# Optimization experiments

Hardware: AMD Instinct MI355X
Metric: run time of the kernel (lower is better)

The kernel has to match this reference:

```python
import jax, jax.numpy as jnp
import numpy as np

B, C, H, W = 64, 64, 56, 56
MID = 2 * C  # two output nodes concatenated
EPS = 1e-5


def _conv1x1(x, w):
    # x: [B,C,H,W], w: [O,C] (1x1 conv kernel squeezed)
    return jnp.einsum('bchw,oc->bohw', x, w)


def _bn(x, g, b, m, v):
    # eval-mode BatchNorm2d with running stats
    sc = g * jax.lax.rsqrt(v + EPS)
    return x * sc[None, :, None, None] + (b - m * sc)[None, :, None, None]


def _maxpool3(x):
    # MaxPool2d(kernel=3, stride=1, padding=1)
    return jax.lax.reduce_window(x, -jnp.inf, jax.lax.max,
                                 (1, 1, 3, 3), (1, 1, 1, 1),
                                 [(0, 0), (0, 0), (1, 1), (1, 1)])


def _avgpool3(x):
    # AvgPool2d(kernel=3, stride=1, padding=1), count_include_pad=True -> /9
    s = jax.lax.reduce_window(x, 0.0, jax.lax.add,
                              (1, 1, 3, 3), (1, 1, 1, 1),
                              [(0, 0), (0, 0), (1, 1), (1, 1)])
    return s * (1.0 / 9.0)


def setup_inputs() -> dict:
    key = jax.random.key(0)
    ks = jax.random.split(key, 11)
    x = jax.random.normal(ks[0], (B, C, H, W), dtype=jnp.float32)
    w1 = jax.random.normal(ks[1], (C, C), dtype=jnp.float32) * 0.1
    w2 = jax.random.normal(ks[2], (C, MID), dtype=jnp.float32) * 0.1
    bn1_g = 1.0 + 0.1 * jax.random.normal(ks[3], (C,), dtype=jnp.float32)
    bn1_b = 0.1 * jax.random.normal(ks[4], (C,), dtype=jnp.float32)
    bn1_m = 0.1 * jax.random.normal(ks[5], (C,), dtype=jnp.float32)
    bn1_v = jax.random.uniform(ks[6], (C,), minval=0.5, maxval=1.5, dtype=jnp.float32)
    bn2_g = 1.0 + 0.1 * jax.random.normal(ks[7], (C,), dtype=jnp.float32)
    bn2_b = 0.1 * jax.random.normal(ks[8], (C,), dtype=jnp.float32)
    bn2_m = 0.1 * jax.random.normal(ks[9], (C,), dtype=jnp.float32)
    bn2_v = jax.random.uniform(ks[10], (C,), minval=0.5, maxval=1.5, dtype=jnp.float32)
    return dict(x=x, w1=w1, w2=w2,
                bn1_g=bn1_g, bn1_b=bn1_b, bn1_m=bn1_m, bn1_v=bn1_v,
                bn2_g=bn2_g, bn2_b=bn2_b, bn2_m=bn2_m, bn2_v=bn2_v)


def reference(x, w1, w2, bn1_g, bn1_b, bn1_m, bn1_v, bn2_g, bn2_b, bn2_m, bn2_v):
    # DAG g = [[[0,1],[1,2]], [[4,3],[3]], [[5,3],[3,100]], [[4,3],[100]]]
    # topoSort order: [0, 2, 1, 3]; output nodes (ordered): [2, 3]
    node0 = jax.nn.relu(_bn(_conv1x1(x, w1), bn1_g, bn1_b, bn1_m, bn1_v))
    node1 = _maxpool3(node0)            # op type 4, pred {0}
    node2 = _avgpool3(node0)            # op type 5, pred {0}
    node3 = _maxpool3(node1) + _maxpool3(node2)  # op type 4, preds {1,2}, summed
    cat = jnp.concatenate([node2, node3], axis=1)  # [B, 2C, H, W]
    out = jax.nn.relu(_bn(_conv1x1(cat, w2), bn2_g, bn2_b, bn2_m, bn2_v))
    return out
```

## Files before the change

### kernel.cpp

```cpp
#include <hip/hip_runtime.h>
#include <cstddef>

#define EPS 1e-5f
static constexpr int Bn = 64, Cn = 64, Hn = 56, Wn = 56, HWn = Hn * Wn;

typedef __attribute__((ext_vector_type(8))) short short8;
typedef __attribute__((ext_vector_type(8))) unsigned short ushort8;
typedef __attribute__((ext_vector_type(4))) float floatx4;
typedef __attribute__((ext_vector_type(16))) float floatx16;
typedef __attribute__((ext_vector_type(4))) unsigned int uintx4;
typedef __attribute__((ext_vector_type(2))) unsigned int uintx2;

__device__ __forceinline__ unsigned pack_rne(float a, float b) {
    unsigned ua = __float_as_uint(a), ub = __float_as_uint(b);
    ua = ua + 0x7fffu + ((ua >> 16) & 1u);
    ub = ub + 0x7fffu + ((ub >> 16) & 1u);
    return __builtin_amdgcn_perm(ub, ua, 0x07060302);
}
__device__ __forceinline__ unsigned pack_trunc(float a, float b) {
    return __builtin_amdgcn_perm(__float_as_uint(b), __float_as_uint(a), 0x07060302);
}
__device__ __forceinline__ ushort8 pmax(ushort8 a, ushort8 b) {
    return __builtin_elementwise_max(a, b);
}
__device__ __forceinline__ float bf_lo(unsigned u) { return __uint_as_float(u << 16); }
__device__ __forceinline__ float bf_hi(unsigned u) { return __uint_as_float(u & 0xffff0000u); }


__global__ __launch_bounds__(256) void k1_conv1(
    const float* __restrict__ x, const float* __restrict__ w1,
    const float* __restrict__ bg, const float* __restrict__ bb,
    const float* __restrict__ bm, const float* __restrict__ bv,
    unsigned short* __restrict__ node0)
{
    __shared__ float scs[64], shs[64];
    const int tid = threadIdx.x;
    if (tid < 64) {
        float sc = bg[tid] * rsqrtf(bv[tid] + EPS);
        scs[tid] = sc;
        shs[tid] = bb[tid] - bm[tid] * sc;
    }
    __syncthreads();
    const int lane = tid & 63;
    const int wv   = tid >> 6;
    const int m    = lane & 15;
    const int quad = lane >> 4;

    short8 afr[4][2];
    float shv[16];
    #pragma unroll
    for (int t = 0; t < 4; ++t) {
        const float sc = scs[t * 16 + m];
        #pragma unroll
        for (int kk = 0; kk < 2; ++kk) {
            const float* wp = w1 + (t * 16 + m) * 64 + kk * 32 + quad * 8;
            floatx4 f0 = *(const floatx4*)wp;
            floatx4 f1 = *(const floatx4*)(wp + 4);
            uintx4 u;
            u.x = pack_rne(f0[0] * sc, f0[1] * sc);
            u.y = pack_rne(f0[2] * sc, f0[3] * sc);
            u.z = pack_rne(f1[0] * sc, f1[1] * sc);
            u.w = pack_rne(f1[2] * sc, f1[3] * sc);
            afr[t][kk] = *(short8*)&u;
        }
        #pragma unroll
        for (int i = 0; i < 4; ++i) shv[t * 4 + i] = shs[t * 16 + quad * 4 + i];
    }

    #pragma unroll 1
    for (int tt = 0; tt < 4; ++tt) {
        const long P0 = (long)blockIdx.x * 256 + tt * 64;
        const int b = (int)(P0 / HWn);
        const int p0 = (int)(P0 - (long)b * HWn);
        const int p = p0 + wv * 16 + m;

        floatx4 acc[4];
        #pragma unroll
        for (int t = 0; t < 4; ++t) acc[t] = (floatx4){0.f, 0.f, 0.f, 0.f};

        #pragma unroll
        for (int kk = 0; kk < 2; ++kk) {
            float xv[8];
            #pragma unroll
            for (int j = 0; j < 8; ++j)
                xv[j] = x[(size_t)(b * 64 + kk * 32 + quad * 8 + j) * HWn + p];
            uintx4 u;
            u.x = pack_trunc(xv[0], xv[1]);
            u.y = pack_trunc(xv[2], xv[3]);
            u.z = pack_trunc(xv[4], xv[5]);
            u.w = pack_trunc(xv[6], xv[7]);
            short8 bfr = *(short8*)&u;
            #pragma unroll
            for (int t = 0; t < 4; ++t)
                acc[t] = __builtin_amdgcn_mfma_f32_16x16x32_bf16(afr[t][kk], bfr, acc[t], 0, 0, 0);
        }

        const int chunkbase = (quad >> 1);
        const int j0 = (quad & 1) * 4;
        #pragma unroll
        for (int t = 0; t < 4; ++t) {
            float v0 = acc[t][0] + shv[t * 4 + 0]; v0 = v0 > 0.f ? v0 : 0.f;
            float v1 = acc[t][1] + shv[t * 4 + 1]; v1 = v1 > 0.f ? v1 : 0.f;
            float v2 = acc[t][2] + shv[t * 4 + 2]; v2 = v2 > 0.f ? v2 : 0.f;
            float v3 = acc[t][3] + shv[t * 4 + 3]; v3 = v3 > 0.f ? v3 : 0.f;
            uintx2 st;
            st.x = pack_rne(v0, v1);
            st.y = pack_rne(v2, v3);
            int chunk = t * 2 + chunkbase;
            *(uintx2*)(node0 + ((size_t)(b * 8 + chunk) * HWn + p0 + wv * 16 + m) * 8 + j0) = st;
        }
    }
}

__global__ __launch_bounds__(256) void k2_pools(
    const unsigned short* __restrict__ node0, unsigned short* __restrict__ cat)
{
    const int tid = threadIdx.x;
    const int lane = tid & 63;
    const int wv = tid >> 6;
    const int bid = blockIdx.x;
    const int half = bid & 1;
    const int band = (bid >> 1) % 7;
    const int b = bid / 14;
    const int chunk = half * 4 + wv;
    const int lo = band * 8;
    const int col = lane;
    const bool act = col < Wn;
    const unsigned short* base = node0 + ((size_t)(b * 8 + chunk) * HWn) * 8;
    unsigned short* cavg = cat + ((size_t)(b * 16 + chunk) * HWn) * 8;
    unsigned short* cmax = cat + ((size_t)(b * 16 + 8 + chunk) * HWn) * 8;

    const ushort8 zz = (ushort8)0;
    float hs1[8], hs2[8];
    ushort8 h5a = zz, h5b = zz, h5c = zz, h5d = zz, nh1 = zz, nh2 = zz;
    #pragma unroll
    for (int j = 0; j < 8; ++j) hs1[j] = hs2[j] = 0.f;

    #pragma unroll
    for (int r = lo - 2; r <= lo + 9; ++r) {
        ushort8 d[5];
        #pragma unroll
        for (int dd = 0; dd < 5; ++dd) {
            int cc = col + dd - 2;
            bool ok = act && ((unsigned)cc < (unsigned)Wn) && ((unsigned)r < (unsigned)Hn);
            d[dd] = ok ? *(const ushort8*)(base + (size_t)(r * Wn + cc) * 8) : zz;
        }
        ushort8 hm5 = pmax(pmax(pmax(d[0], d[1]), pmax(d[2], d[3])), d[4]);
        ushort8 m5 = pmax(pmax(pmax(h5a, h5b), pmax(h5c, h5d)), hm5);
        h5a = h5b; h5b = h5c; h5c = h5d; h5d = hm5;

        const uintx4 ul = *(const uintx4*)&d[1];
        const uintx4 uv = *(const uintx4*)&d[2];
        const uintx4 ur = *(const uintx4*)&d[3];
        float a2[8];
        const int r2 = r - 1, r3 = r - 2;
        const bool v2 = (unsigned)r2 < (unsigned)Hn;
        #pragma unroll
        for (int w = 0; w < 4; ++w) {
            float l0 = bf_lo(ul[w]), l1 = bf_hi(ul[w]);
            float c0 = bf_lo(uv[w]), c1 = bf_hi(uv[w]);
            float r0 = bf_lo(ur[w]), r1 = bf_hi(ur[w]);
            float hsum0 = l0 + c0 + r0;
            float hsum1 = l1 + c1 + r1;
            a2[w * 2 + 0] = v2 ? (hs2[w * 2 + 0] + hs1[w * 2 + 0] + hsum0) * (1.f / 9.f) : 0.f;
            a2[w * 2 + 1] = v2 ? (hs2[w * 2 + 1] + hs1[w * 2 + 1] + hsum1) * (1.f / 9.f) : 0.f;
            hs2[w * 2 + 0] = hs1[w * 2 + 0]; hs1[w * 2 + 0] = hsum0;
            hs2[w * 2 + 1] = hs1[w * 2 + 1]; hs1[w * 2 + 1] = hsum1;
        }
        uintx4 ap;
        ap.x = pack_rne(a2[0], a2[1]);
        ap.y = pack_rne(a2[2], a2[3]);
        ap.z = pack_rne(a2[4], a2[5]);
        ap.w = pack_rne(a2[6], a2[7]);
        uintx4 al, ar;
        #pragma unroll
        for (int w = 0; w < 4; ++w) {
            unsigned u = ap[w];
            unsigned lu = __shfl_up(u, 1);
            unsigned ru = __shfl_down(u, 1);
            al[w] = (lane == 0) ? 0u : lu;
            ar[w] = (lane == 63) ? 0u : ru;
        }
        ushort8 nh = pmax(pmax(*(ushort8*)&al, *(ushort8*)&ap), *(ushort8*)&ar);
        ushort8 m3 = pmax(pmax(nh2, nh1), nh);
        nh2 = nh1; nh1 = nh;

        if (act && r2 >= lo && r2 < lo + 8)
            *(uintx4*)(cavg + (size_t)(r2 * Wn + col) * 8) = ap;
        if (act && r3 >= lo && r3 < lo + 8) {
            const uintx4 u5 = *(const uintx4*)&m5;
            const uintx4 u3 = *(const uintx4*)&m3;
            uintx4 st;
            #pragma unroll
            for (int w = 0; w < 4; ++w)
                st[w] = pack_rne(bf_lo(u5[w]) + bf_lo(u3[w]), bf_hi(u5[w]) + bf_hi(u3[w]));
            *(uintx4*)(cmax + (size_t)(r3 * Wn + col) * 8) = st;
        }
    }
}

__global__ __launch_bounds__(256) void k3_conv2(
    const unsigned short* __restrict__ cat, const float* __restrict__ w2,
    const float* __restrict__ bg, const float* __restrict__ bb,
    const float* __restrict__ bm, const float* __restrict__ bv,
    float* __restrict__ out)
{
    __shared__ unsigned short wl[1024 * 8];
    __shared__ float scs[64], shs[64];
    const int tid = threadIdx.x;
    if (tid < 64) {
        float sc = bg[tid] * rsqrtf(bv[tid] + EPS);
        scs[tid] = sc;
        shs[tid] = bb[tid] - bm[tid] * sc;
    }
    #pragma unroll
    for (int q = 0; q < 4; ++q) {
        int ci = tid * 4 + q;
        int lane_ = ci & 63, tk = ci >> 6;
        int t = tk >> 3, kt = tk & 7, n_ = lane_ & 31, h_ = lane_ >> 5;
        const float* wp = w2 + (t * 32 + n_) * 128 + kt * 16 + h_ * 8;
        floatx4 f0 = *(const floatx4*)wp;
        floatx4 f1 = *(const floatx4*)(wp + 4);
        uintx4 u;
        u.x = pack_rne(f0[0], f0[1]);
        u.y = pack_rne(f0[2], f0[3]);
        u.z = pack_rne(f1[0], f1[1]);
        u.w = pack_rne(f1[2], f1[3]);
        *(uintx4*)(wl + (size_t)ci * 8) = u;
    }
    __syncthreads();

    const int lane = tid & 63;
    const int wv = tid >> 6;
    const int n = lane & 31;
    const int h = lane >> 5;

    short8 afr[2][8];
    #pragma unroll
    for (int t = 0; t < 2; ++t)
        #pragma unroll
        for (int kt = 0; kt < 8; ++kt)
            afr[t][kt] = *(const short8*)(wl + ((size_t)((t * 8 + kt) * 64 + lane)) * 8);

    #pragma unroll 1
    for (int s = 0; s < 2; ++s) {
        const int tile = (blockIdx.x * 4 + wv) * 2 + s;
        const int b = tile / 98;
        const int p0 = (tile - b * 98) * 32;

        floatx16 acc0, acc1;
        #pragma unroll
        for (int i = 0; i < 16; ++i) { acc0[i] = 0.f; acc1[i] = 0.f; }

        #pragma unroll
        for (int kt = 0; kt < 8; ++kt) {
            short8 bfr = *(const short8*)(cat + ((size_t)(b * 16 + kt * 2 + h) * HWn + p0 + n) * 8);
            acc0 = __builtin_amdgcn_mfma_f32_32x32x16_bf16(afr[0][kt], bfr, acc0, 0, 0, 0);
            acc1 = __builtin_amdgcn_mfma_f32_32x32x16_bf16(afr[1][kt], bfr, acc1, 0, 0, 0);
        }

        float* ob = out + (size_t)b * 64 * HWn + p0 + n;
        #pragma unroll
        for (int r = 0; r < 16; ++r) {
            int o = (r & 3) + 8 * (r >> 2) + 4 * h;
            float v0 = fmaf(acc0[r], scs[o], shs[o]);
            ob[(size_t)o * HWn] = v0 > 0.f ? v0 : 0.f;
            float v1 = fmaf(acc1[r], scs[o + 32], shs[o + 32]);
            ob[(size_t)(o + 32) * HWn] = v1 > 0.f ? v1 : 0.f;
        }
    }
}

extern "C" void kernel_launch(void* const* d_in, const int* in_sizes, int n_in,
                              void* d_out, int out_size, void* d_ws, size_t ws_size,
                              hipStream_t stream)
{
    const float* x   = (const float*)d_in[0];
    const float* w1  = (const float*)d_in[1];
    const float* w2  = (const float*)d_in[2];
    const float* b1g = (const float*)d_in[3];
    const float* b1b = (const float*)d_in[4];
    const float* b1m = (const float*)d_in[5];
    const float* b1v = (const float*)d_in[6];
    const float* b2g = (const float*)d_in[7];
    const float* b2b = (const float*)d_in[8];
    const float* b2m = (const float*)d_in[9];
    const float* b2v = (const float*)d_in[10];

    float* out = (float*)d_out;
    unsigned short* node0 = (unsigned short*)d_ws;
    unsigned short* cat   = node0 + (size_t)Bn * HWn * 64;

    k1_conv1<<<dim3(784), dim3(256), 0, stream>>>(x, w1, b1g, b1b, b1m, b1v, node0);
    k2_pools<<<dim3(Bn * 14), dim3(256), 0, stream>>>(node0, cat);
    k3_conv2<<<dim3(784), dim3(256), 0, stream>>>(cat, w2, b2g, b2b, b2m, b2v, out);
}
```

Before: 165.4 us.

## Fuse pooling stage into second 1x1 conv through shared-memory concat tile

Merges the pooling kernel and the second conv kernel into one kernel. Each 512-thread block computes the avg and max-sum pools for a 4-row band of one image across all 8 channel chunks, writing the concatenated activations into a padded LDS tile. Seven waves then run the MFMA conv directly from LDS. This drops the global round trip of the 128-channel cat tensor and one launch. In exchange, the halo rows are recomputed per smaller band (8 rows loaded for 4 output rows), the LDS footprint is large, and one wave idles during the conv phase.

```diff
diff --git a/kernel.cpp b/kernel.cpp
--- a/kernel.cpp
+++ b/kernel.cpp
@@ -3,6 +3,7 @@
 
 #define EPS 1e-5f
 static constexpr int Bn = 64, Cn = 64, Hn = 56, Wn = 56, HWn = Hn * Wn;
+static constexpr int CSTR = 136;
 
 typedef __attribute__((ext_vector_type(8))) short short8;
 typedef __attribute__((ext_vector_type(8))) unsigned short ushort8;
@@ -112,99 +113,13 @@
     }
 }
 
-__global__ __launch_bounds__(256) void k2_pools(
-    const unsigned short* __restrict__ node0, unsigned short* __restrict__ cat)
-{
-    const int tid = threadIdx.x;
-    const int lane = tid & 63;
-    const int wv = tid >> 6;
-    const int bid = blockIdx.x;
-    const int half = bid & 1;
-    const int band = (bid >> 1) % 7;
-    const int b = bid / 14;
-    const int chunk = half * 4 + wv;
-    const int lo = band * 8;
-    const int col = lane;
-    const bool act = col < Wn;
-    const unsigned short* base = node0 + ((size_t)(b * 8 + chunk) * HWn) * 8;
-    unsigned short* cavg = cat + ((size_t)(b * 16 + chunk) * HWn) * 8;
-    unsigned short* cmax = cat + ((size_t)(b * 16 + 8 + chunk) * HWn) * 8;
-
-    const ushort8 zz = (ushort8)0;
-    float hs1[8], hs2[8];
-    ushort8 h5a = zz, h5b = zz, h5c = zz, h5d = zz, nh1 = zz, nh2 = zz;
-    #pragma unroll
-    for (int j = 0; j < 8; ++j) hs1[j] = hs2[j] = 0.f;
-
-    #pragma unroll
-    for (int r = lo - 2; r <= lo + 9; ++r) {
-        ushort8 d[5];
-        #pragma unroll
-        for (int dd = 0; dd < 5; ++dd) {
-            int cc = col + dd - 2;
-            bool ok = act && ((unsigned)cc < (unsigned)Wn) && ((unsigned)r < (unsigned)Hn);
-            d[dd] = ok ? *(const ushort8*)(base + (size_t)(r * Wn + cc) * 8) : zz;
-        }
-        ushort8 hm5 = pmax(pmax(pmax(d[0], d[1]), pmax(d[2], d[3])), d[4]);
-        ushort8 m5 = pmax(pmax(pmax(h5a, h5b), pmax(h5c, h5d)), hm5);
-        h5a = h5b; h5b = h5c; h5c = h5d; h5d = hm5;
-
-        const uintx4 ul = *(const uintx4*)&d[1];
-        const uintx4 uv = *(const uintx4*)&d[2];
-        const uintx4 ur = *(const uintx4*)&d[3];
-        float a2[8];
-        const int r2 = r - 1, r3 = r - 2;
-        const bool v2 = (unsigned)r2 < (unsigned)Hn;
-        #pragma unroll
-        for (int w = 0; w < 4; ++w) {
-            float l0 = bf_lo(ul[w]), l1 = bf_hi(ul[w]);
-            float c0 = bf_lo(uv[w]), c1 = bf_hi(uv[w]);
-            float r0 = bf_lo(ur[w]), r1 = bf_hi(ur[w]);
-            float hsum0 = l0 + c0 + r0;
-            float hsum1 = l1 + c1 + r1;
-            a2[w * 2 + 0] = v2 ? (hs2[w * 2 + 0] + hs1[w * 2 + 0] + hsum0) * (1.f / 9.f) : 0.f;
-            a2[w * 2 + 1] = v2 ? (hs2[w * 2 + 1] + hs1[w * 2 + 1] + hsum1) * (1.f / 9.f) : 0.f;
-            hs2[w * 2 + 0] = hs1[w * 2 + 0]; hs1[w * 2 + 0] = hsum0;
-            hs2[w * 2 + 1] = hs1[w * 2 + 1]; hs1[w * 2 + 1] = hsum1;
-        }
-        uintx4 ap;
-        ap.x = pack_rne(a2[0], a2[1]);
-        ap.y = pack_rne(a2[2], a2[3]);
-        ap.z = pack_rne(a2[4], a2[5]);
-        ap.w = pack_rne(a2[6], a2[7]);
-        uintx4 al, ar;
-        #pragma unroll
-        for (int w = 0; w < 4; ++w) {
-            unsigned u = ap[w];
-            unsigned lu = __shfl_up(u, 1);
-            unsigned ru = __shfl_down(u, 1);
-            al[w] = (lane == 0) ? 0u : lu;
-            ar[w] = (lane == 63) ? 0u : ru;
-        }
-        ushort8 nh = pmax(pmax(*(ushort8*)&al, *(ushort8*)&ap), *(ushort8*)&ar);
-        ushort8 m3 = pmax(pmax(nh2, nh1), nh);
-        nh2 = nh1; nh1 = nh;
-
-        if (act && r2 >= lo && r2 < lo + 8)
-            *(uintx4*)(cavg + (size_t)(r2 * Wn + col) * 8) = ap;
-        if (act && r3 >= lo && r3 < lo + 8) {
-            const uintx4 u5 = *(const uintx4*)&m5;
-            const uintx4 u3 = *(const uintx4*)&m3;
-            uintx4 st;
-            #pragma unroll
-            for (int w = 0; w < 4; ++w)
-                st[w] = pack_rne(bf_lo(u5[w]) + bf_lo(u3[w]), bf_hi(u5[w]) + bf_hi(u3[w]));
-            *(uintx4*)(cmax + (size_t)(r3 * Wn + col) * 8) = st;
-        }
-    }
-}
-
-__global__ __launch_bounds__(256) void k3_conv2(
-    const unsigned short* __restrict__ cat, const float* __restrict__ w2,
+__global__ __launch_bounds__(512, 4) void k23_fused(
+    const unsigned short* __restrict__ node0, const float* __restrict__ w2,
     const float* __restrict__ bg, const float* __restrict__ bb,
     const float* __restrict__ bm, const float* __restrict__ bv,
     float* __restrict__ out)
 {
+    __shared__ unsigned short ct[224 * CSTR];
     __shared__ unsigned short wl[1024 * 8];
     __shared__ float scs[64], shs[64];
     const int tid = threadIdx.x;
@@ -214,8 +129,8 @@
         shs[tid] = bb[tid] - bm[tid] * sc;
     }
     #pragma unroll
-    for (int q = 0; q < 4; ++q) {
-        int ci = tid * 4 + q;
+    for (int q = 0; q < 2; ++q) {
+        int ci = tid * 2 + q;
         int lane_ = ci & 63, tk = ci >> 6;
         int t = tk >> 3, kt = tk & 7, n_ = lane_ & 31, h_ = lane_ >> 5;
         const float* wp = w2 + (t * 32 + n_) * 128 + kt * 16 + h_ * 8;
@@ -228,10 +143,88 @@
         u.w = pack_rne(f1[2], f1[3]);
         *(uintx4*)(wl + (size_t)ci * 8) = u;
     }
-    __syncthreads();
 
     const int lane = tid & 63;
     const int wv = tid >> 6;
+    const int b = blockIdx.x / 14;
+    const int band = blockIdx.x % 14;
+    const int lo = band * 4;
+    const int col = lane;
+    const bool act = col < Wn;
+    const unsigned short* base = node0 + ((size_t)(b * 8 + wv) * HWn) * 8;
+
+    {
+        const ushort8 zz = (ushort8)0;
+        float hs1[8], hs2[8];
+        ushort8 h5a = zz, h5b = zz, h5c = zz, h5d = zz, nh1 = zz, nh2 = zz;
+        #pragma unroll
+        for (int j = 0; j < 8; ++j) hs1[j] = hs2[j] = 0.f;
+
+        #pragma unroll
+        for (int r = lo - 2; r <= lo + 5; ++r) {
+            ushort8 d[5];
+            #pragma unroll
+            for (int dd = 0; dd < 5; ++dd) {
+                int cc = col + dd - 2;
+                bool ok = act && ((unsigned)cc < (unsigned)Wn) && ((unsigned)r < (unsigned)Hn);
+                d[dd] = ok ? *(const ushort8*)(base + (size_t)(r * Wn + cc) * 8) : zz;
+            }
+            ushort8 hm5 = pmax(pmax(pmax(d[0], d[1]), pmax(d[2], d[3])), d[4]);
+            ushort8 m5 = pmax(pmax(pmax(h5a, h5b), pmax(h5c, h5d)), hm5);
+            h5a = h5b; h5b = h5c; h5c = h5d; h5d = hm5;
+
+            const uintx4 ul = *(const uintx4*)&d[1];
+            const uintx4 uv = *(const uintx4*)&d[2];
+            const uintx4 ur = *(const uintx4*)&d[3];
+            float a2[8];
+            const int r2 = r - 1, r3 = r - 2;
+            const bool v2 = (unsigned)r2 < (unsigned)Hn;
+            #pragma unroll
+            for (int w = 0; w < 4; ++w) {
+                float hsum0 = bf_lo(ul[w]) + bf_lo(uv[w]) + bf_lo(ur[w]);
+                float hsum1 = bf_hi(ul[w]) + bf_hi(uv[w]) + bf_hi(ur[w]);
+                a2[w * 2 + 0] = v2 ? (hs2[w * 2 + 0] + hs1[w * 2 + 0] + hsum0) * (1.f / 9.f) : 0.f;
+                a2[w * 2 + 1] = v2 ? (hs2[w * 2 + 1] + hs1[w * 2 + 1] + hsum1) * (1.f / 9.f) : 0.f;
+                hs2[w * 2 + 0] = hs1[w * 2 + 0]; hs1[w * 2 + 0] = hsum0;
+                hs2[w * 2 + 1] = hs1[w * 2 + 1]; hs1[w * 2 + 1] = hsum1;
+            }
+            uintx4 ap;
+            ap.x = pack_rne(a2[0], a2[1]);
+            ap.y = pack_rne(a2[2], a2[3]);
+            ap.z = pack_rne(a2[4], a2[5]);
+            ap.w = pack_rne(a2[6], a2[7]);
+            uintx4 al, ar;
+            #pragma unroll
+            for (int w = 0; w < 4; ++w) {
+                unsigned u = ap[w];
+                unsigned lu = __shfl_up(u, 1);
+                unsigned ru = __shfl_down(u, 1);
+                al[w] = (lane == 0) ? 0u : lu;
+                ar[w] = (lane == 63) ? 0u : ru;
+            }
+            ushort8 nh = pmax(pmax(*(ushort8*)&al, *(ushort8*)&ap), *(ushort8*)&ar);
+            ushort8 m3 = pmax(pmax(nh2, nh1), nh);
+            nh2 = nh1; nh1 = nh;
+
+            if (act && r2 >= lo && r2 < lo + 4) {
+                int px = (r2 - lo) * Wn + col;
+                *(uintx4*)(ct + (size_t)px * CSTR + wv * 8) = ap;
+            }
+            if (act && r3 >= lo && r3 < lo + 4) {
+                const uintx4 u5 = *(const uintx4*)&m5;
+                const uintx4 u3 = *(const uintx4*)&m3;
+                uintx4 st;
+                #pragma unroll
+                for (int w = 0; w < 4; ++w)
+                    st[w] = pack_rne(bf_lo(u5[w]) + bf_lo(u3[w]), bf_hi(u5[w]) + bf_hi(u3[w]));
+                int px = (r3 - lo) * Wn + col;
+                *(uintx4*)(ct + (size_t)px * CSTR + 64 + wv * 8) = st;
+            }
+        }
+    }
+    __syncthreads();
+
+    if (wv >= 7) return;
     const int n = lane & 31;
     const int h = lane >> 5;
 
@@ -242,32 +235,26 @@
         for (int kt = 0; kt < 8; ++kt)
             afr[t][kt] = *(const short8*)(wl + ((size_t)((t * 8 + kt) * 64 + lane)) * 8);
 
-    #pragma unroll 1
-    for (int s = 0; s < 2; ++s) {
-        const int tile = (blockIdx.x * 4 + wv) * 2 + s;
-        const int b = tile / 98;
-        const int p0 = (tile - b * 98) * 32;
-
-        floatx16 acc0, acc1;
-        #pragma unroll
-        for (int i = 0; i < 16; ++i) { acc0[i] = 0.f; acc1[i] = 0.f; }
-
-        #pragma unroll
-        for (int kt = 0; kt < 8; ++kt) {
-            short8 bfr = *(const short8*)(cat + ((size_t)(b * 16 + kt * 2 + h) * HWn + p0 + n) * 8);
-            acc0 = __builtin_amdgcn_mfma_f32_32x32x16_bf16(afr[0][kt], bfr, acc0, 0, 0, 0);
-            acc1 = __builtin_amdgcn_mfma_f32_32x32x16_bf16(afr[1][kt], bfr, acc1, 0, 0, 0);
-        }
-
-        float* ob = out + (size_t)b * 64 * HWn + p0 + n;
-        #pragma unroll
-        for (int r = 0; r < 16; ++r) {
-            int o = (r & 3) + 8 * (r >> 2) + 4 * h;
-            float v0 = fmaf(acc0[r], scs[o], shs[o]);
-            ob[(size_t)o * HWn] = v0 > 0.f ? v0 : 0.f;
-            float v1 = fmaf(acc1[r], scs[o + 32], shs[o + 32]);
-            ob[(size_t)(o + 32) * HWn] = v1 > 0.f ? v1 : 0.f;
-        }
+    const int px0 = wv * 32;
+    floatx16 acc0, acc1;
+    #pragma unroll
+    for (int i = 0; i < 16; ++i) { acc0[i] = 0.f; acc1[i] = 0.f; }
+
+    #pragma unroll
+    for (int kt = 0; kt < 8; ++kt) {
+        short8 bfr = *(const short8*)(ct + (size_t)(px0 + n) * CSTR + kt * 16 + h * 8);
+        acc0 = __builtin_amdgcn_mfma_f32_32x32x16_bf16(afr[0][kt], bfr, acc0, 0, 0, 0);
+        acc1 = __builtin_amdgcn_mfma_f32_32x32x16_bf16(afr[1][kt], bfr, acc1, 0, 0, 0);
+    }
+
+    float* ob = out + (size_t)b * 64 * HWn + lo * Wn + px0 + n;
+    #pragma unroll
+    for (int r = 0; r < 16; ++r) {
+        int o = (r & 3) + 8 * (r >> 2) + 4 * h;
+        float v0 = fmaf(acc0[r], scs[o], shs[o]);
+        ob[(size_t)o * HWn] = v0 > 0.f ? v0 : 0.f;
+        float v1 = fmaf(acc1[r], scs[o + 32], shs[o + 32]);
+        ob[(size_t)(o + 32) * HWn] = v1 > 0.f ? v1 : 0.f;
     }
 }
 
@@ -289,9 +276,7 @@
 
     float* out = (float*)d_out;
     unsigned short* node0 = (unsigned short*)d_ws;
-    unsigned short* cat   = node0 + (size_t)Bn * HWn * 64;
 
     k1_conv1<<<dim3(784), dim3(256), 0, stream>>>(x, w1, b1g, b1b, b1m, b1v, node0);
-    k2_pools<<<dim3(Bn * 14), dim3(256), 0, stream>>>(node0, cat);
-    k3_conv2<<<dim3(784), dim3(256), 0, stream>>>(cat, w2, b2g, b2b, b2m, b2v, out);
-}
+    k23_fused<<<dim3(Bn * 14), dim3(512), 0, stream>>>(node0, w2, b2g, b2b, b2m, b2v, out);
+}
```

Measured after the change: 170.6 us. 1.03x slower.

## Stage conv1 input through double-buffered LDS and prefetch rows in pooling kernel

Applied to the files above, without the earlier changes.

Conv1 now loads each 64-pixel x tile with coalesced float4 global loads into a register stage, transposes it into a padded LDS buffer, and double-buffers so the next tile's global load overlaps the current tile's MFMA work. This replaces the earlier strided scalar per-channel global loads. The pooling kernel software-prefetches the next row's five neighbour loads before processing the current row. The conv2 tile loop is also fully unrolled. The cost is extra LDS use, barriers, and register pressure.

```diff
diff --git a/kernel.cpp b/kernel.cpp
--- a/kernel.cpp
+++ b/kernel.cpp
@@ -3,6 +3,7 @@
 
 #define EPS 1e-5f
 static constexpr int Bn = 64, Cn = 64, Hn = 56, Wn = 56, HWn = Hn * Wn;
+static constexpr int XS = 65;
 
 typedef __attribute__((ext_vector_type(8))) short short8;
 typedef __attribute__((ext_vector_type(8))) unsigned short ushort8;
@@ -33,6 +34,7 @@
     const float* __restrict__ bm, const float* __restrict__ bv,
     unsigned short* __restrict__ node0)
 {
+    __shared__ float xs[2][64 * XS];
     __shared__ float scs[64], shs[64];
     const int tid = threadIdx.x;
     if (tid < 64) {
@@ -45,6 +47,7 @@
     const int wv   = tid >> 6;
     const int m    = lane & 15;
     const int quad = lane >> 4;
+    const int qoff = quad * 8;
 
     short8 afr[4][2];
     float shv[16];
@@ -53,7 +56,7 @@
         const float sc = scs[t * 16 + m];
         #pragma unroll
         for (int kk = 0; kk < 2; ++kk) {
-            const float* wp = w1 + (t * 16 + m) * 64 + kk * 32 + quad * 8;
+            const float* wp = w1 + (t * 16 + m) * 64 + kk * 32 + qoff;
             floatx4 f0 = *(const floatx4*)wp;
             floatx4 f1 = *(const floatx4*)(wp + 4);
             uintx4 u;
@@ -67,12 +70,39 @@
         for (int i = 0; i < 4; ++i) shv[t * 4 + i] = shs[t * 16 + quad * 4 + i];
     }
 
-    #pragma unroll 1
+    floatx4 stg[4];
+    auto ldtile = [&](int tt) {
+        const int P = blockIdx.x * 256 + tt * 64;
+        const int b = P / HWn, p0 = P - b * HWn;
+        #pragma unroll
+        for (int q = 0; q < 4; ++q) {
+            int idx = q * 256 + tid;
+            int c = idx >> 4, f = idx & 15;
+            stg[q] = *(const floatx4*)(x + (size_t)(b * 64 + c) * HWn + p0 + f * 4);
+        }
+    };
+    auto sttile = [&](int buf) {
+        #pragma unroll
+        for (int q = 0; q < 4; ++q) {
+            int idx = q * 256 + tid;
+            int c = idx >> 4, f = idx & 15;
+            #pragma unroll
+            for (int k = 0; k < 4; ++k)
+                xs[buf][(f * 4 + k) * XS + c] = stg[q][k];
+        }
+    };
+
+    ldtile(0);
+    sttile(0);
+
+    #pragma unroll
     for (int tt = 0; tt < 4; ++tt) {
-        const long P0 = (long)blockIdx.x * 256 + tt * 64;
-        const int b = (int)(P0 / HWn);
-        const int p0 = (int)(P0 - (long)b * HWn);
-        const int p = p0 + wv * 16 + m;
+        __syncthreads();
+        if (tt < 3) ldtile(tt + 1);
+
+        const int P = blockIdx.x * 256 + tt * 64;
+        const int b = P / HWn, p0 = P - b * HWn;
+        const float* xr = &xs[tt & 1][(wv * 16 + m) * XS];
 
         floatx4 acc[4];
         #pragma unroll
@@ -80,15 +110,14 @@
 
         #pragma unroll
         for (int kk = 0; kk < 2; ++kk) {
-            float xv[8];
+            float f[8];
             #pragma unroll
-            for (int j = 0; j < 8; ++j)
-                xv[j] = x[(size_t)(b * 64 + kk * 32 + quad * 8 + j) * HWn + p];
+            for (int j = 0; j < 8; ++j) f[j] = xr[kk * 32 + qoff + j];
             uintx4 u;
-            u.x = pack_trunc(xv[0], xv[1]);
-            u.y = pack_trunc(xv[2], xv[3]);
-            u.z = pack_trunc(xv[4], xv[5]);
-            u.w = pack_trunc(xv[6], xv[7]);
+            u.x = pack_trunc(f[0], f[1]);
+            u.y = pack_trunc(f[2], f[3]);
+            u.z = pack_trunc(f[4], f[5]);
+            u.w = pack_trunc(f[6], f[7]);
             short8 bfr = *(short8*)&u;
             #pragma unroll
             for (int t = 0; t < 4; ++t)
@@ -109,6 +138,8 @@
             int chunk = t * 2 + chunkbase;
             *(uintx2*)(node0 + ((size_t)(b * 8 + chunk) * HWn + p0 + wv * 16 + m) * 8 + j0) = st;
         }
+
+        if (tt < 3) sttile((tt + 1) & 1);
     }
 }
 
@@ -131,20 +162,29 @@
     unsigned short* cmax = cat + ((size_t)(b * 16 + 8 + chunk) * HWn) * 8;
 
     const ushort8 zz = (ushort8)0;
-    float hs1[8], hs2[8];
-    ushort8 h5a = zz, h5b = zz, h5c = zz, h5d = zz, nh1 = zz, nh2 = zz;
-    #pragma unroll
-    for (int j = 0; j < 8; ++j) hs1[j] = hs2[j] = 0.f;
-
-    #pragma unroll
-    for (int r = lo - 2; r <= lo + 9; ++r) {
-        ushort8 d[5];
+    auto load5 = [&](int r, ushort8* d) {
         #pragma unroll
         for (int dd = 0; dd < 5; ++dd) {
             int cc = col + dd - 2;
             bool ok = act && ((unsigned)cc < (unsigned)Wn) && ((unsigned)r < (unsigned)Hn);
             d[dd] = ok ? *(const ushort8*)(base + (size_t)(r * Wn + cc) * 8) : zz;
         }
+    };
+
+    float hs1[8], hs2[8];
+    ushort8 h5a = zz, h5b = zz, h5c = zz, h5d = zz, nh1 = zz, nh2 = zz;
+    #pragma unroll
+    for (int j = 0; j < 8; ++j) hs1[j] = hs2[j] = 0.f;
+
+    ushort8 d[5];
+    load5(lo - 2, d);
+
+    #pragma unroll
+    for (int i = 0; i < 12; ++i) {
+        const int r = lo - 2 + i;
+        ushort8 dn[5];
+        if (i < 11) load5(r + 1, dn);
+
         ushort8 hm5 = pmax(pmax(pmax(d[0], d[1]), pmax(d[2], d[3])), d[4]);
         ushort8 m5 = pmax(pmax(pmax(h5a, h5b), pmax(h5c, h5d)), hm5);
         h5a = h5b; h5b = h5c; h5c = h5d; h5d = hm5;
@@ -157,11 +197,8 @@
         const bool v2 = (unsigned)r2 < (unsigned)Hn;
         #pragma unroll
         for (int w = 0; w < 4; ++w) {
-            float l0 = bf_lo(ul[w]), l1 = bf_hi(ul[w]);
-            float c0 = bf_lo(uv[w]), c1 = bf_hi(uv[w]);
-            float r0 = bf_lo(ur[w]), r1 = bf_hi(ur[w]);
-            float hsum0 = l0 + c0 + r0;
-            float hsum1 = l1 + c1 + r1;
+            float hsum0 = bf_lo(ul[w]) + bf_lo(uv[w]) + bf_lo(ur[w]);
+            float hsum1 = bf_hi(ul[w]) + bf_hi(uv[w]) + bf_hi(ur[w]);
             a2[w * 2 + 0] = v2 ? (hs2[w * 2 + 0] + hs1[w * 2 + 0] + hsum0) * (1.f / 9.f) : 0.f;
             a2[w * 2 + 1] = v2 ? (hs2[w * 2 + 1] + hs1[w * 2 + 1] + hsum1) * (1.f / 9.f) : 0.f;
             hs2[w * 2 + 0] = hs1[w * 2 + 0]; hs1[w * 2 + 0] = hsum0;
@@ -196,6 +233,8 @@
                 st[w] = pack_rne(bf_lo(u5[w]) + bf_lo(u3[w]), bf_hi(u5[w]) + bf_hi(u3[w]));
             *(uintx4*)(cmax + (size_t)(r3 * Wn + col) * 8) = st;
         }
+        #pragma unroll
+        for (int dd = 0; dd < 5; ++dd) d[dd] = dn[dd];
     }
 }
 
@@ -242,7 +281,7 @@
         for (int kt = 0; kt < 8; ++kt)
             afr[t][kt] = *(const short8*)(wl + ((size_t)((t * 8 + kt) * 64 + lane)) * 8);
 
-    #pragma unroll 1
+    #pragma unroll
     for (int s = 0; s < 2; ++s) {
         const int tile = (blockIdx.x * 4 + wv) * 2 + s;
         const int b = tile / 98;
```

After: 159.9 us. -3.3%, faster.
